# Kernel optimization log

Hardware: AMD Instinct MI355X
Metric: run time of the kernel (lower is better)

Reference implementation:

```python
import jax, jax.numpy as jnp
import numpy as np

MARGIN = 0.2  # TripletMarginLoss margin and TripletMarginMiner margin


def setup_inputs() -> dict:
    key = jax.random.key(0)
    k1, k2 = jax.random.split(key)
    embeddings = jax.random.normal(k1, (384, 256), dtype=jnp.float32)
    labels = jax.random.randint(k2, (384,), 0, 32)
    return {"embeddings": embeddings, "labels": labels}


def _pairwise_l2(e):
    # Euclidean distance matrix with sqrt-safe gradient at zero.
    sq = jnp.sum(e * e, axis=1)
    d2 = jnp.maximum(sq[:, None] + sq[None, :] - 2.0 * (e @ e.T), 0.0)
    pos = d2 > 0.0
    return jnp.sqrt(jnp.where(pos, d2, 1.0)) * pos


def reference(embeddings, labels):
    # pytorch-metric-learning LpDistance defaults: normalize_embeddings=True, p=2
    e = embeddings / jnp.maximum(
        jnp.linalg.norm(embeddings, axis=1, keepdims=True), 1e-12
    )
    D = _pairwise_l2(e)  # [B, B]
    n = D.shape[0]

    same = labels[:, None] == labels[None, :]
    eye = jnp.eye(n, dtype=bool)
    pos_mask = same & ~eye   # valid (anchor, positive) pairs
    neg_mask = ~same         # valid (anchor, negative) pairs

    ap = D[:, :, None]       # dist(anchor, positive), broadcast over negative
    an = D[:, None, :]       # dist(anchor, negative), broadcast over positive
    tm = an - ap             # miner's triplet_margin (is_inverted=False)

    valid = pos_mask[:, :, None] & neg_mask[:, None, :]     # [B, B, B]
    # semihard miner: 0 < an - ap <= margin
    semihard = valid & (tm > 0.0) & (tm <= MARGIN)

    # TripletMarginLoss per-triplet loss: relu(ap - an + margin) = relu(margin - tm)
    losses = jnp.where(semihard, jnp.maximum(MARGIN - tm, 0.0), 0.0)

    # AvgNonZeroReducer: mean over strictly-positive losses (0 if none)
    nz = jnp.sum(losses > 0.0)
    total = jnp.sum(losses)
    return jnp.where(nz > 0, total / jnp.maximum(nz, 1).astype(total.dtype), 0.0)
```

## Files before the change

### kernel.cpp

```cpp
#include <hip/hip_runtime.h>

#define N        384
#define DIM      256
#define D4       (DIM / 4)
#define MARGIN_F 0.2f
#define NANCH    2
#define NBLK     (N / NANCH)
#define NTHR     384
#define NWAVE    (NTHR / 64)
#define MAXPOS   64


__global__ __launch_bounds__(64) void norm_kernel(
    const float* __restrict__ emb, float4* __restrict__ eTv,
    float* __restrict__ sqn)
{
    const int row  = blockIdx.x;
    const int lane = threadIdx.x;

    const float4 v = ((const float4*)emb)[row * D4 + lane];
    float s = v.x*v.x + v.y*v.y + v.z*v.z + v.w*v.w;
    #pragma unroll
    for (int off = 32; off > 0; off >>= 1) s += __shfl_down(s, off, 64);
    const float tot = __shfl(s, 0, 64);

    const float inv = 1.0f / fmaxf(sqrtf(tot), 1e-12f);
    float4 vn;
    vn.x = v.x * inv; vn.y = v.y * inv; vn.z = v.z * inv; vn.w = v.w * inv;
    eTv[lane * N + row] = vn;

    if (lane == 0) sqn[row] = tot * inv * inv;
}

__global__ __launch_bounds__(NTHR) void fused_kernel(
    const float4* __restrict__ eTv, const float* __restrict__ sqn,
    const int* __restrict__ labels,
    float* __restrict__ accum_sum, unsigned int* __restrict__ accum_cnt,
    unsigned int* __restrict__ done_cnt, float* __restrict__ out)
{
    const int i0   = blockIdx.x * NANCH;
    const int tid  = threadIdx.x;
    const int wave = tid >> 6, lane = tid & 63;

    __shared__ float4 ei4[NANCH][D4];
    __shared__ float  sqa[NANCH];
    __shared__ float  Drow[NANCH][N];
    __shared__ int    lab[N];
    __shared__ int    posList[NANCH][MAXPOS];
    __shared__ int    posCnt[NANCH];
    __shared__ float        sredS[NWAVE];
    __shared__ unsigned int sredC[NWAVE];

    if (tid < NANCH * D4) {
        const int a = tid >> 6, k4 = tid & (D4 - 1);
        ei4[a][k4] = eTv[k4 * N + (i0 + a)];
    }
    if (tid < NANCH) { sqa[tid] = sqn[i0 + tid]; posCnt[tid] = 0; }
    lab[tid] = labels[tid];
    __syncthreads();

    float acc0 = 0.0f, acc1 = 0.0f;
    #pragma unroll 8
    for (int k4 = 0; k4 < D4; ++k4) {
        const float4 v  = eTv[k4 * N + tid];
        const float4 a0 = ei4[0][k4];
        const float4 a1 = ei4[1][k4];
        acc0 += v.x*a0.x + v.y*a0.y + v.z*a0.z + v.w*a0.w;
        acc1 += v.x*a1.x + v.y*a1.y + v.z*a1.z + v.w*a1.w;
    }
    const float sqj = sqn[tid];
    {
        float d2 = fmaxf(sqa[0] + sqj - 2.0f * acc0, 0.0f);
        Drow[0][tid] = (d2 > 0.0f) ? sqrtf(d2) : 0.0f;
        d2       = fmaxf(sqa[1] + sqj - 2.0f * acc1, 0.0f);
        Drow[1][tid] = (d2 > 0.0f) ? sqrtf(d2) : 0.0f;
    }
    __syncthreads();

    const int lj = lab[tid];
    #pragma unroll
    for (int a = 0; a < NANCH; ++a) {
        const int ia = i0 + a;
        if (lj == lab[ia] && tid != ia)
            posList[a][atomicAdd(&posCnt[a], 1)] = tid;
    }
    __syncthreads();

    float        lsum = 0.0f;
    unsigned int lcnt = 0u;
    #pragma unroll
    for (int a = 0; a < NANCH; ++a) {
        const int   li = lab[i0 + a];
        const float dk = Drow[a][tid];
        if (lj != li) {
            const int np = posCnt[a];
            for (int p = 0; p < np; ++p) {
                const float tm = dk - Drow[a][posList[a][p]];
                if (tm > 0.0f && tm <= MARGIN_F) {
                    const float l = MARGIN_F - tm;
                    lsum += l;
                    if (l > 0.0f) lcnt++;
                }
            }
        }
    }

    #pragma unroll
    for (int off = 32; off > 0; off >>= 1) {
        lsum += __shfl_down(lsum, off, 64);
        lcnt += __shfl_down(lcnt, off, 64);
    }
    if (lane == 0) { sredS[wave] = lsum; sredC[wave] = lcnt; }
    __syncthreads();

    if (tid == 0) {
        float        S = 0.0f;
        unsigned int C = 0u;
        #pragma unroll
        for (int w = 0; w < NWAVE; ++w) { S += sredS[w]; C += sredC[w]; }
        if (S != 0.0f || C != 0u) {
            atomicAdd(accum_sum, S);
            atomicAdd(accum_cnt, C);
        }
        __threadfence();
        const unsigned int prev = atomicAdd(done_cnt, 1);
        if (prev == NBLK - 1) {
            const float        Sall = atomicAdd(accum_sum, 0.0f);
            const unsigned int Call = atomicAdd(accum_cnt, 0u);
            out[0] = (Call > 0u) ? (Sall / (float)Call) : 0.0f;
        }
    }
}

extern "C" void kernel_launch(void* const* d_in, const int* in_sizes, int n_in,
                              void* d_out, int out_size, void* d_ws, size_t ws_size,
                              hipStream_t stream) {
    const float* emb    = (const float*)d_in[0];
    const int*   labels = (const int*)d_in[1];
    float*       out    = (float*)d_out;

    float*        accum_sum = (float*)d_ws;
    unsigned int* accum_cnt = (unsigned int*)accum_sum + 1;
    unsigned int* done_cnt  = (unsigned int*)accum_sum + 2;
    float4*       eTv = (float4*)((char*)d_ws + 16);
    float*        sqn = (float*)((char*)d_ws + 16 + (size_t)N * DIM * 4);

    hipMemsetAsync(d_ws, 0, 16, stream);
    norm_kernel<<<N, 64, 0, stream>>>(emb, eTv, sqn);
    fused_kernel<<<NBLK, NTHR, 0, stream>>>(eTv, sqn, labels,
                                            accum_sum, accum_cnt, done_cnt, out);
}
```

Baseline: 77.38 us.

## Drop memset launch and replace global atomics with per-block partials

```diff
diff --git a/kernel.cpp b/kernel.cpp
--- a/kernel.cpp
+++ b/kernel.cpp
@@ -13,10 +13,16 @@
 
 __global__ __launch_bounds__(64) void norm_kernel(
     const float* __restrict__ emb, float4* __restrict__ eTv,
-    float* __restrict__ sqn)
+    float* __restrict__ sqn, float* __restrict__ psum,
+    unsigned int* __restrict__ pcnt, unsigned int* __restrict__ done_cnt)
 {
     const int row  = blockIdx.x;
     const int lane = threadIdx.x;
+
+    if (lane == 0) {
+        if (row < NBLK) { psum[row] = 0.0f; pcnt[row] = 0u; }
+        if (row == 0)   { *done_cnt = 0u; }
+    }
 
     const float4 v = ((const float4*)emb)[row * D4 + lane];
     float s = v.x*v.x + v.y*v.y + v.z*v.z + v.w*v.w;
@@ -35,7 +41,7 @@
 __global__ __launch_bounds__(NTHR) void fused_kernel(
     const float4* __restrict__ eTv, const float* __restrict__ sqn,
     const int* __restrict__ labels,
-    float* __restrict__ accum_sum, unsigned int* __restrict__ accum_cnt,
+    float* __restrict__ psum, unsigned int* __restrict__ pcnt,
     unsigned int* __restrict__ done_cnt, float* __restrict__ out)
 {
     const int i0   = blockIdx.x * NANCH;
@@ -50,6 +56,7 @@
     __shared__ int    posCnt[NANCH];
     __shared__ float        sredS[NWAVE];
     __shared__ unsigned int sredC[NWAVE];
+    __shared__ int    isLast;
 
     if (tid < NANCH * D4) {
         const int a = tid >> 6, k4 = tid & (D4 - 1);
@@ -60,7 +67,7 @@
     __syncthreads();
 
     float acc0 = 0.0f, acc1 = 0.0f;
-    #pragma unroll 8
+    #pragma unroll 16
     for (int k4 = 0; k4 < D4; ++k4) {
         const float4 v  = eTv[k4 * N + tid];
         const float4 a0 = ei4[0][k4];
@@ -119,14 +126,34 @@
         #pragma unroll
         for (int w = 0; w < NWAVE; ++w) { S += sredS[w]; C += sredC[w]; }
         if (S != 0.0f || C != 0u) {
-            atomicAdd(accum_sum, S);
-            atomicAdd(accum_cnt, C);
+            atomicAdd(&psum[blockIdx.x], S);
+            atomicAdd(&pcnt[blockIdx.x], C);
         }
         __threadfence();
         const unsigned int prev = atomicAdd(done_cnt, 1);
-        if (prev == NBLK - 1) {
-            const float        Sall = atomicAdd(accum_sum, 0.0f);
-            const unsigned int Call = atomicAdd(accum_cnt, 0u);
+        isLast = (prev == NBLK - 1) ? 1 : 0;
+    }
+    __syncthreads();
+
+    if (isLast) {
+        float        s = 0.0f;
+        unsigned int c = 0u;
+        if (tid < NBLK) {
+            s = atomicAdd(&psum[tid], 0.0f);
+            c = atomicAdd(&pcnt[tid], 0u);
+        }
+        #pragma unroll
+        for (int off = 32; off > 0; off >>= 1) {
+            s += __shfl_down(s, off, 64);
+            c += __shfl_down(c, off, 64);
+        }
+        if (lane == 0) { sredS[wave] = s; sredC[wave] = c; }
+        __syncthreads();
+        if (tid == 0) {
+            float        Sall = 0.0f;
+            unsigned int Call = 0u;
+            #pragma unroll
+            for (int w = 0; w < NWAVE; ++w) { Sall += sredS[w]; Call += sredC[w]; }
             out[0] = (Call > 0u) ? (Sall / (float)Call) : 0.0f;
         }
     }
@@ -139,14 +166,13 @@
     const int*   labels = (const int*)d_in[1];
     float*       out    = (float*)d_out;
 
-    float*        accum_sum = (float*)d_ws;
-    unsigned int* accum_cnt = (unsigned int*)accum_sum + 1;
-    unsigned int* done_cnt  = (unsigned int*)accum_sum + 2;
-    float4*       eTv = (float4*)((char*)d_ws + 16);
-    float*        sqn = (float*)((char*)d_ws + 16 + (size_t)N * DIM * 4);
+    unsigned int* done_cnt = (unsigned int*)d_ws;
+    float*        psum     = (float*)((char*)d_ws + 16);
+    unsigned int* pcnt     = (unsigned int*)((char*)d_ws + 16 + 768);
+    float4*       eTv      = (float4*)((char*)d_ws + 1552);
+    float*        sqn      = (float*)((char*)d_ws + 1552 + (size_t)N * DIM * 4);
 
-    hipMemsetAsync(d_ws, 0, 16, stream);
-    norm_kernel<<<N, 64, 0, stream>>>(emb, eTv, sqn);
+    norm_kernel<<<N, 64, 0, stream>>>(emb, eTv, sqn, psum, pcnt, done_cnt);
     fused_kernel<<<NBLK, NTHR, 0, stream>>>(eTv, sqn, labels,
-                                            accum_sum, accum_cnt, done_cnt, out);
+                                            psum, pcnt, done_cnt, out);
 }
```

After: 79.98 us. 1.03x slower.

## Fuse normalization into triplet kernel with wave-per-row dot products

Applied to the files above, without the earlier changes.

```diff
diff --git a/kernel.cpp b/kernel.cpp
--- a/kernel.cpp
+++ b/kernel.cpp
@@ -8,33 +8,12 @@
 #define NBLK     (N / NANCH)
 #define NTHR     384
 #define NWAVE    (NTHR / 64)
+#define ROWSPW   (N / NWAVE)
 #define MAXPOS   64
 
 
-__global__ __launch_bounds__(64) void norm_kernel(
-    const float* __restrict__ emb, float4* __restrict__ eTv,
-    float* __restrict__ sqn)
-{
-    const int row  = blockIdx.x;
-    const int lane = threadIdx.x;
-
-    const float4 v = ((const float4*)emb)[row * D4 + lane];
-    float s = v.x*v.x + v.y*v.y + v.z*v.z + v.w*v.w;
-    #pragma unroll
-    for (int off = 32; off > 0; off >>= 1) s += __shfl_down(s, off, 64);
-    const float tot = __shfl(s, 0, 64);
-
-    const float inv = 1.0f / fmaxf(sqrtf(tot), 1e-12f);
-    float4 vn;
-    vn.x = v.x * inv; vn.y = v.y * inv; vn.z = v.z * inv; vn.w = v.w * inv;
-    eTv[lane * N + row] = vn;
-
-    if (lane == 0) sqn[row] = tot * inv * inv;
-}
-
-__global__ __launch_bounds__(NTHR) void fused_kernel(
-    const float4* __restrict__ eTv, const float* __restrict__ sqn,
-    const int* __restrict__ labels,
+__global__ __launch_bounds__(NTHR) void triplet_kernel(
+    const float* __restrict__ emb, const int* __restrict__ labels,
     float* __restrict__ accum_sum, unsigned int* __restrict__ accum_cnt,
     unsigned int* __restrict__ done_cnt, float* __restrict__ out)
 {
@@ -51,29 +30,48 @@
     __shared__ float        sredS[NWAVE];
     __shared__ unsigned int sredC[NWAVE];
 
-    if (tid < NANCH * D4) {
-        const int a = tid >> 6, k4 = tid & (D4 - 1);
-        ei4[a][k4] = eTv[k4 * N + (i0 + a)];
+    lab[tid] = labels[tid];
+    if (tid < NANCH) posCnt[tid] = 0;
+    if (wave < NANCH) {
+        const float4 v = ((const float4*)emb)[(i0 + wave) * D4 + lane];
+        float s = v.x*v.x + v.y*v.y + v.z*v.z + v.w*v.w;
+        #pragma unroll
+        for (int m = 1; m < 64; m <<= 1) s += __shfl_xor(s, m, 64);
+        const float inv = 1.0f / fmaxf(sqrtf(s), 1e-12f);
+        float4 vn;
+        vn.x = v.x*inv; vn.y = v.y*inv; vn.z = v.z*inv; vn.w = v.w*inv;
+        ei4[wave][lane] = vn;
+        if (lane == 0) sqa[wave] = s * inv * inv;
     }
-    if (tid < NANCH) { sqa[tid] = sqn[i0 + tid]; posCnt[tid] = 0; }
-    lab[tid] = labels[tid];
     __syncthreads();
 
-    float acc0 = 0.0f, acc1 = 0.0f;
-    #pragma unroll 8
-    for (int k4 = 0; k4 < D4; ++k4) {
-        const float4 v  = eTv[k4 * N + tid];
-        const float4 a0 = ei4[0][k4];
-        const float4 a1 = ei4[1][k4];
-        acc0 += v.x*a0.x + v.y*a0.y + v.z*a0.z + v.w*a0.w;
-        acc1 += v.x*a1.x + v.y*a1.y + v.z*a1.z + v.w*a1.w;
-    }
-    const float sqj = sqn[tid];
-    {
-        float d2 = fmaxf(sqa[0] + sqj - 2.0f * acc0, 0.0f);
-        Drow[0][tid] = (d2 > 0.0f) ? sqrtf(d2) : 0.0f;
-        d2       = fmaxf(sqa[1] + sqj - 2.0f * acc1, 0.0f);
-        Drow[1][tid] = (d2 > 0.0f) ? sqrtf(d2) : 0.0f;
+    const float4 a0 = ei4[0][lane];
+    const float4 a1 = ei4[1][lane];
+    const float  sq0 = sqa[0], sq1 = sqa[1];
+    const float4* __restrict__ embr = (const float4*)emb;
+    const int jbase = wave * ROWSPW;
+
+    #pragma unroll 4
+    for (int r = 0; r < ROWSPW; ++r) {
+        const int j = jbase + r;
+        const float4 v = embr[j * D4 + lane];
+        float vv  = v.x*v.x  + v.y*v.y  + v.z*v.z  + v.w*v.w;
+        float rd0 = v.x*a0.x + v.y*a0.y + v.z*a0.z + v.w*a0.w;
+        float rd1 = v.x*a1.x + v.y*a1.y + v.z*a1.z + v.w*a1.w;
+        #pragma unroll
+        for (int m = 1; m < 64; m <<= 1) {
+            vv  += __shfl_xor(vv,  m, 64);
+            rd0 += __shfl_xor(rd0, m, 64);
+            rd1 += __shfl_xor(rd1, m, 64);
+        }
+        const float inv = 1.0f / fmaxf(sqrtf(vv), 1e-12f);
+        const float sqj = vv * inv * inv;
+        if (lane < NANCH) {
+            const float rd = (lane == 0) ? rd0 : rd1;
+            const float sa = (lane == 0) ? sq0 : sq1;
+            const float d2 = fmaxf(sa + sqj - 2.0f * (rd * inv), 0.0f);
+            Drow[lane][j] = (d2 > 0.0f) ? sqrtf(d2) : 0.0f;
+        }
     }
     __syncthreads();
 
@@ -142,11 +140,8 @@
     float*        accum_sum = (float*)d_ws;
     unsigned int* accum_cnt = (unsigned int*)accum_sum + 1;
     unsigned int* done_cnt  = (unsigned int*)accum_sum + 2;
-    float4*       eTv = (float4*)((char*)d_ws + 16);
-    float*        sqn = (float*)((char*)d_ws + 16 + (size_t)N * DIM * 4);
 
     hipMemsetAsync(d_ws, 0, 16, stream);
-    norm_kernel<<<N, 64, 0, stream>>>(emb, eTv, sqn);
-    fused_kernel<<<NBLK, NTHR, 0, stream>>>(eTv, sqn, labels,
-                                            accum_sum, accum_cnt, done_cnt, out);
+    triplet_kernel<<<NBLK, NTHR, 0, stream>>>(emb, labels,
+                                              accum_sum, accum_cnt, done_cnt, out);
 }
```

Measured after the change: 104.4 us. 1.35x slower.

## Double block threads to split dot-product K dimension and anchors across halves

Applied to the files above, without the earlier changes.

```diff
diff --git a/kernel.cpp b/kernel.cpp
--- a/kernel.cpp
+++ b/kernel.cpp
@@ -3,10 +3,11 @@
 #define N        384
 #define DIM      256
 #define D4       (DIM / 4)
+#define KH       (D4 / 2)
 #define MARGIN_F 0.2f
 #define NANCH    2
 #define NBLK     (N / NANCH)
-#define NTHR     384
+#define NTHR     (2 * N)
 #define NWAVE    (NTHR / 64)
 #define MAXPOS   64
 
@@ -41,9 +42,12 @@
     const int i0   = blockIdx.x * NANCH;
     const int tid  = threadIdx.x;
     const int wave = tid >> 6, lane = tid & 63;
+    const int kgrp = (tid >= N) ? 1 : 0;
+    const int col  = tid - kgrp * N;
 
     __shared__ float4 ei4[NANCH][D4];
     __shared__ float  sqa[NANCH];
+    __shared__ float  pacc[NANCH][N];
     __shared__ float  Drow[NANCH][N];
     __shared__ int    lab[N];
     __shared__ int    posList[NANCH][MAXPOS];
@@ -56,44 +60,50 @@
         ei4[a][k4] = eTv[k4 * N + (i0 + a)];
     }
     if (tid < NANCH) { sqa[tid] = sqn[i0 + tid]; posCnt[tid] = 0; }
-    lab[tid] = labels[tid];
+    if (tid < N) lab[tid] = labels[tid];
     __syncthreads();
 
     float acc0 = 0.0f, acc1 = 0.0f;
+    const int kbase = kgrp * KH;
     #pragma unroll 8
-    for (int k4 = 0; k4 < D4; ++k4) {
-        const float4 v  = eTv[k4 * N + tid];
+    for (int k = 0; k < KH; ++k) {
+        const int k4 = kbase + k;
+        const float4 v  = eTv[k4 * N + col];
         const float4 a0 = ei4[0][k4];
         const float4 a1 = ei4[1][k4];
         acc0 += v.x*a0.x + v.y*a0.y + v.z*a0.z + v.w*a0.w;
         acc1 += v.x*a1.x + v.y*a1.y + v.z*a1.z + v.w*a1.w;
     }
-    const float sqj = sqn[tid];
-    {
-        float d2 = fmaxf(sqa[0] + sqj - 2.0f * acc0, 0.0f);
-        Drow[0][tid] = (d2 > 0.0f) ? sqrtf(d2) : 0.0f;
-        d2       = fmaxf(sqa[1] + sqj - 2.0f * acc1, 0.0f);
-        Drow[1][tid] = (d2 > 0.0f) ? sqrtf(d2) : 0.0f;
-    }
+    if (kgrp == 1) { pacc[0][col] = acc0; pacc[1][col] = acc1; }
     __syncthreads();
 
-    const int lj = lab[tid];
-    #pragma unroll
-    for (int a = 0; a < NANCH; ++a) {
-        const int ia = i0 + a;
-        if (lj == lab[ia] && tid != ia)
-            posList[a][atomicAdd(&posCnt[a], 1)] = tid;
+    if (kgrp == 0) {
+        acc0 += pacc[0][col];
+        acc1 += pacc[1][col];
+        const float sqj = sqn[col];
+        float d2 = fmaxf(sqa[0] + sqj - 2.0f * acc0, 0.0f);
+        Drow[0][col] = (d2 > 0.0f) ? sqrtf(d2) : 0.0f;
+        d2       = fmaxf(sqa[1] + sqj - 2.0f * acc1, 0.0f);
+        Drow[1][col] = (d2 > 0.0f) ? sqrtf(d2) : 0.0f;
+    } else {
+        const int lj = lab[col];
+        #pragma unroll
+        for (int a = 0; a < NANCH; ++a) {
+            const int ia = i0 + a;
+            if (lj == lab[ia] && col != ia)
+                posList[a][atomicAdd(&posCnt[a], 1)] = col;
+        }
     }
     __syncthreads();
 
     float        lsum = 0.0f;
     unsigned int lcnt = 0u;
-    #pragma unroll
-    for (int a = 0; a < NANCH; ++a) {
+    {
+        const int   a  = kgrp;
         const int   li = lab[i0 + a];
-        const float dk = Drow[a][tid];
-        if (lj != li) {
-            const int np = posCnt[a];
+        if (lab[col] != li) {
+            const float dk = Drow[a][col];
+            const int   np = posCnt[a];
             for (int p = 0; p < np; ++p) {
                 const float tm = dk - Drow[a][posList[a][p]];
                 if (tm > 0.0f && tm <= MARGIN_F) {
```

Measured after the change: 74.74 us. 1.04x faster.
